# Kernel optimization log

Hardware: AMD Instinct MI355X
Metric: run time of the kernel (lower is better)

Reference implementation:

```python
import jax, jax.numpy as jnp
import numpy as np

NMS_RADIUS = 4   # default_config['nms_radius']
MAX_KP = 256     # default_config['max_keypoints']


def _conv2d(x, w, b):
    y = jax.lax.conv_general_dilated(x, w, (1, 1), [(1, 1), (1, 1)],
                                     dimension_numbers=('NCHW', 'OIHW', 'NCHW'))
    return y + b[None, :, None, None]


def _conv1d(x, w, b, pad):
    y = jax.lax.conv_general_dilated(x, w, (1,), [(pad, pad)],
                                     dimension_numbers=('NCH', 'OIH', 'NCH'))
    return y + b[None, :, None]


def _maxpool(x, r):
    k = 2 * r + 1
    return jax.lax.reduce_window(x, -jnp.inf, jax.lax.max,
                                 (1, k, k), (1, 1, 1), [(0, 0), (r, r), (r, r)])


def _simple_nms(scores, r):
    zeros = jnp.zeros_like(scores)
    max_mask = scores == _maxpool(scores, r)
    for _ in range(2):
        supp_mask = _maxpool(max_mask.astype(scores.dtype), r) > 0
        supp_scores = jnp.where(supp_mask, zeros, scores)
        new_max_mask = supp_scores == _maxpool(supp_scores, r)
        max_mask = max_mask | (new_max_mask & ~supp_mask)
    return jnp.where(max_mask, scores, zeros)


def _affine_grid(theta, H, W):
    # F.affine_grid with align_corners=False
    xs = (jnp.arange(W, dtype=theta.dtype) + 0.5) * (2.0 / W) - 1.0
    ys = (jnp.arange(H, dtype=theta.dtype) + 0.5) * (2.0 / H) - 1.0
    Y, X = jnp.meshgrid(ys, xs, indexing='ij')  # (H, W)
    gx = theta[:, 0, 0, None, None] * X + theta[:, 0, 1, None, None] * Y + theta[:, 0, 2, None, None]
    gy = theta[:, 1, 0, None, None] * X + theta[:, 1, 1, None, None] * Y + theta[:, 1, 2, None, None]
    return jnp.stack([gx, gy], axis=-1)  # (N, H, W, 2)


def _grid_sample(img, grid):
    # F.grid_sample, bilinear, padding_mode='zeros', align_corners=False
    N, C, H, W = img.shape
    ix = ((grid[..., 0] + 1.0) * W - 1.0) * 0.5
    iy = ((grid[..., 1] + 1.0) * H - 1.0) * 0.5
    x0 = jnp.floor(ix); y0 = jnp.floor(iy)
    x1 = x0 + 1.0;      y1 = y0 + 1.0

    def gather(xi, yi):
        valid = (xi >= 0) & (xi <= W - 1) & (yi >= 0) & (yi <= H - 1)
        xc = jnp.clip(xi, 0, W - 1).astype(jnp.int32)
        yc = jnp.clip(yi, 0, H - 1).astype(jnp.int32)
        v = jax.vmap(lambda im, y, x: im[:, y, x])(img, yc, xc)  # (N, C, H, W)
        return v * valid[:, None].astype(img.dtype)

    wa = ((x1 - ix) * (y1 - iy))[:, None]
    wb = ((ix - x0) * (y1 - iy))[:, None]
    wc = ((x1 - ix) * (iy - y0))[:, None]
    wd = ((ix - x0) * (iy - y0))[:, None]
    return (gather(x0, y0) * wa + gather(x1, y0) * wb +
            gather(x0, y1) * wc + gather(x1, y1) * wd)


def setup_inputs() -> dict:
    key = jax.random.key(0)
    ks = jax.random.split(key, 12)
    L, C, H, W = 4, 256, 128, 256
    Cd = C // 2
    s = 0.02
    return {
        'feats':   jax.random.normal(ks[0], (L, C, H, W), jnp.float32),
        'convS_w': jax.random.normal(ks[1], (1, C, 3, 3), jnp.float32) * s,
        'convS_b': jax.random.normal(ks[2], (1,), jnp.float32) * s,
        'convD_w': jax.random.normal(ks[3], (Cd, C, 3, 3), jnp.float32) * s,
        'convD_b': jax.random.normal(ks[4], (Cd,), jnp.float32) * s,
        'proj_w':  jax.random.normal(ks[5], (Cd, Cd, 3), jnp.float32) * s,
        'proj_b':  jax.random.normal(ks[6], (Cd,), jnp.float32) * s,
        'projS_w': jax.random.normal(ks[7], (Cd, Cd, 1), jnp.float32) * s,
        'projS_b': jax.random.normal(ks[8], (Cd,), jnp.float32) * s,
        'final_w': jax.random.normal(ks[9], (3, Cd, 1), jnp.float32) * s,
        'final_b': jax.random.normal(ks[10], (3,), jnp.float32) * s,
    }


def reference(feats, convS_w, convS_b, convD_w, convD_b,
              proj_w, proj_b, projS_w, projS_b, final_w, final_b):
    L, C, H, W = feats.shape
    scores = jax.nn.sigmoid(_conv2d(feats, convS_w, convS_b))[:, 0]   # (L, H, W)
    desc = jax.nn.relu(_conv2d(feats, convD_w, convD_b))               # (L, C//2, H, W)

    scores = _simple_nms(scores, NMS_RADIUS).reshape(L, -1)
    _, top_idx = jax.lax.top_k(scores, MAX_KP)                         # (L, K)

    # F.normalize(p=2, dim=1)
    norm = jnp.sqrt(jnp.sum(desc * desc, axis=1, keepdims=True))
    desc = desc / jnp.maximum(norm, 1e-12)
    desc = desc.reshape(L, desc.shape[1], -1)                          # (L, Cd, HW)
    desc = jnp.take_along_axis(desc, top_idx[:, None, :], axis=2)      # (L, Cd, K)

    # AttentionalGNN: out = desc + (desc + message) = 2*desc + message
    Cd = desc.shape[1]
    qkv = jnp.transpose(desc, (2, 0, 1))                               # (K, L, Cd)
    attn = jnp.einsum('knc,kmc->knm', qkv, qkv) / jnp.sqrt(jnp.asarray(Cd, desc.dtype))
    prob = jax.nn.softmax(attn, axis=-1)
    message = jnp.einsum('knm,kmc->knc', prob, qkv)
    desc = 2.0 * desc + jnp.transpose(message, (1, 2, 0))

    desc = jax.nn.relu(_conv1d(desc, proj_w, proj_b, 1))
    s = _conv1d(desc, projS_w, projS_b, 0)
    order = jnp.argsort(-s, axis=-1)                                   # sort descending per channel
    desc = jnp.take_along_axis(desc, order, axis=-1)
    desc = _conv1d(desc, final_w, final_b, 0)                          # (L, 3, K)
    desc = desc - desc[0:1]

    idx = jnp.argmin(jnp.abs(desc), axis=2, keepdims=True)             # (L, 3, 1)
    picked = jnp.take_along_axis(desc, idx, axis=2)[:, :, 0]           # (L, 3)
    # picked * (picked/|picked|) == picked * sign(picked); sign(0)=0 matches the
    # original's nan->0 replacement for the first (zero-difference) sample.
    min_desc = picked * jnp.sign(picked)
    # the original builds t_matrix from Python floats (math.cos), detaching grads
    min_desc = jax.lax.stop_gradient(min_desc)

    th, tx, ty = min_desc[:, 2], min_desc[:, 0], min_desc[:, 1]
    row0 = jnp.stack([jnp.cos(th), -jnp.sin(th), tx], axis=1)
    row1 = jnp.stack([jnp.sin(th), jnp.cos(th), ty], axis=1)
    theta = jnp.stack([row0, row1], axis=1)                            # (L, 2, 3)

    grid = _affine_grid(theta, H, W)
    return _grid_sample(feats, grid)
```

## Files before the change

### kernel.cpp

```cpp
#include <hip/hip_runtime.h>

#define LIMG 4
#define CIN 256
#define HH 128
#define WW 256
#define HW 32768
#define LHW 131072
#define CD 128
#define KP 256
#define CAP 8192
#define NSP 2
#define CPER (CIN/NSP)
#define NINF -3.402823466e38f

__global__ __launch_bounds__(256) void k_chanred(const float* __restrict__ feats,
                                                 const float* __restrict__ wS,
                                                 float* __restrict__ g,
                                                 const float* __restrict__ wD,
                                                 float* __restrict__ wT,
                                                 int* __restrict__ cnt) {
  int bid = blockIdx.x;
  if (bid >= 1024) {
    int i = (bid - 1024) * 256 + threadIdx.x;
    if (i < LIMG) cnt[i] = 0;
    if (i < CD * CIN * 9) {
      int d = i & (CD - 1);
      int j = i >> 7;
      wT[i] = wD[d * (CIN * 9) + j];
    }
    return;
  }
  int gp   = (bid & 511) * 256 + threadIdx.x;
  int half = bid >> 9;
  int l  = gp >> 15;
  int pi = gp & (HW - 1);
  const float* f = feats + (size_t)(l * CIN + half * CPER) * HW + pi;
  const float* w = wS + half * CPER * 9;
  float a0=0,a1=0,a2=0,a3=0,a4=0,a5=0,a6=0,a7=0,a8=0;
  #pragma unroll 4
  for (int c = 0; c < CPER; ++c) {
    float v = f[(size_t)c * HW];
    const float* wc = w + c * 9;
    a0 = fmaf(wc[0], v, a0); a1 = fmaf(wc[1], v, a1); a2 = fmaf(wc[2], v, a2);
    a3 = fmaf(wc[3], v, a3); a4 = fmaf(wc[4], v, a4); a5 = fmaf(wc[5], v, a5);
    a6 = fmaf(wc[6], v, a6); a7 = fmaf(wc[7], v, a7); a8 = fmaf(wc[8], v, a8);
  }
  float* go = g + (size_t)(half * 9) * LHW + gp;
  go[0*(size_t)LHW]=a0; go[1*(size_t)LHW]=a1; go[2*(size_t)LHW]=a2;
  go[3*(size_t)LHW]=a3; go[4*(size_t)LHW]=a4; go[5*(size_t)LHW]=a5;
  go[6*(size_t)LHW]=a6; go[7*(size_t)LHW]=a7; go[8*(size_t)LHW]=a8;
}

__global__ __launch_bounds__(256) void k_scores(const float* __restrict__ g,
                                                const float* __restrict__ bS,
                                                float* __restrict__ scores) {
  int gp = blockIdx.x * 256 + threadIdx.x;
  int l  = gp >> 15;
  int pi = gp & (HW - 1);
  int y = pi >> 8, x = pi & 255;
  float acc = bS[0];
  #pragma unroll
  for (int ky = 0; ky < 3; ++ky) {
    int yy = y + ky - 1;
    if (yy < 0 || yy >= HH) continue;
    #pragma unroll
    for (int kx = 0; kx < 3; ++kx) {
      int xx = x + kx - 1;
      if (xx < 0 || xx >= WW) continue;
      int tap = ky * 3 + kx;
      size_t q = (size_t)l * HW + yy * WW + xx;
      acc += g[(size_t)tap * LHW + q] + g[(size_t)(9 + tap) * LHW + q];
    }
  }
  scores[gp] = 1.0f / (1.0f + expf(-acc));
}

__global__ __launch_bounds__(256) void k_nms01(const float* __restrict__ scores,
                                               float* __restrict__ maskout) {
  __shared__ float sS[32][152];
  __shared__ float buf[32][152];
  __shared__ float sM[24][144];
  __shared__ float ss[16][136];
  __shared__ float smc[8][128];
  int b = blockIdx.x;
  int l  = b >> 5;
  int yt = (b >> 1) & 15;
  int xt = b & 1;
  int y0 = yt * 8;
  int x0 = xt * 128;
  int tid = threadIdx.x;
  const float* sl = scores + (size_t)l * HW;
  if (tid < 152) {
    int gx = x0 - 12 + tid;
    bool vx = (gx >= 0 && gx < WW);
    for (int r = 0; r < 32; ++r) {
      int gy = y0 - 12 + r;
      sS[r][tid] = (vx && gy >= 0 && gy < HH) ? sl[gy * WW + gx] : NINF;
    }
  }
  __syncthreads();
  if (tid < 144) {
    for (int r = 0; r < 32; ++r) {
      float m = sS[r][tid];
      #pragma unroll
      for (int dx = 1; dx <= 8; ++dx) m = fmaxf(m, sS[r][tid + dx]);
      buf[r][tid] = m;
    }
  }
  __syncthreads();
  if (tid < 144) {
    int gx = x0 - 8 + tid;
    bool vx = (gx >= 0 && gx < WW);
    for (int r3 = 0; r3 < 24; ++r3) {
      int gy = y0 - 8 + r3;
      float m = buf[r3][tid];
      #pragma unroll
      for (int t = 1; t < 9; ++t) m = fmaxf(m, buf[r3 + t][tid]);
      sM[r3][tid] = (vx && gy >= 0 && gy < HH && sS[r3 + 4][tid + 4] == m) ? 1.0f : 0.0f;
    }
  }
  __syncthreads();
  if (tid < 136) {
    for (int r3 = 0; r3 < 24; ++r3) {
      float m = sM[r3][tid];
      #pragma unroll
      for (int dx = 1; dx <= 8; ++dx) m = fmaxf(m, sM[r3][tid + dx]);
      buf[r3][tid] = m;
    }
  }
  __syncthreads();
  if (tid < 136) {
    int gx = x0 - 4 + tid;
    bool vx = (gx >= 0 && gx < WW);
    for (int r2 = 0; r2 < 16; ++r2) {
      int gy = y0 - 4 + r2;
      float m = buf[r2][tid];
      #pragma unroll
      for (int t = 1; t < 9; ++t) m = fmaxf(m, buf[r2 + t][tid]);
      bool sm = m > 0.0f;
      bool vin = vx && gy >= 0 && gy < HH;
      ss[r2][tid] = (sm || !vin) ? 0.0f : sS[r2 + 8][tid + 8];
      if (r2 >= 4 && r2 < 12 && tid >= 4 && tid < 132)
        smc[r2 - 4][tid - 4] = sm ? 1.0f : 0.0f;
    }
  }
  __syncthreads();
  if (tid < 128) {
    for (int r2 = 0; r2 < 16; ++r2) {
      float m = ss[r2][tid];
      #pragma unroll
      for (int dx = 1; dx <= 8; ++dx) m = fmaxf(m, ss[r2][tid + dx]);
      buf[r2][tid] = m;
    }
  }
  __syncthreads();
  if (tid < 128) {
    int gx = x0 + tid;
    for (int r = 0; r < 8; ++r) {
      float m = buf[r][tid];
      #pragma unroll
      for (int t = 1; t < 9; ++t) m = fmaxf(m, buf[r + t][tid]);
      bool nm = (ss[r + 4][tid + 4] == m) && (smc[r][tid] == 0.0f);
      float prev = sM[r + 8][tid + 8];
      maskout[l * HW + (y0 + r) * WW + gx] = (prev != 0.0f || nm) ? 1.0f : 0.0f;
    }
  }
}

__global__ __launch_bounds__(256) void k_nms2(const float* __restrict__ maskin,
                                              const float* __restrict__ scores,
                                              float* __restrict__ maskout,
                                              int* __restrict__ cnt,
                                              int* __restrict__ cidx,
                                              float* __restrict__ csc) {
  __shared__ float m24[24][144];
  __shared__ float buf[24][144];
  __shared__ float ss[16][136];
  __shared__ float smc[8][128];
  int b = blockIdx.x;
  int l  = b >> 5;
  int yt = (b >> 1) & 15;
  int xt = b & 1;
  int y0 = yt * 8;
  int x0 = xt * 128;
  int tid = threadIdx.x;
  const float* ml = maskin + (size_t)l * HW;
  const float* sl = scores + (size_t)l * HW;
  if (tid < 144) {
    int gx = x0 - 8 + tid;
    bool vx = (gx >= 0 && gx < WW);
    for (int r = 0; r < 24; ++r) {
      int gy = y0 - 8 + r;
      m24[r][tid] = (vx && gy >= 0 && gy < HH) ? ml[gy * WW + gx] : 0.0f;
    }
  }
  __syncthreads();
  if (tid < 136) {
    for (int r = 0; r < 24; ++r) {
      float m = m24[r][tid];
      #pragma unroll
      for (int dx = 1; dx <= 8; ++dx) m = fmaxf(m, m24[r][tid + dx]);
      buf[r][tid] = m;
    }
  }
  __syncthreads();
  if (tid < 136) {
    int gx = x0 - 4 + tid;
    bool vx = (gx >= 0 && gx < WW);
    for (int r2 = 0; r2 < 16; ++r2) {
      int gy = y0 - 4 + r2;
      float m = buf[r2][tid];
      #pragma unroll
      for (int t = 1; t < 9; ++t) m = fmaxf(m, buf[r2 + t][tid]);
      bool sm = m > 0.0f;
      bool vin = vx && gy >= 0 && gy < HH;
      ss[r2][tid] = (sm || !vin) ? 0.0f : sl[gy * WW + gx];
      if (r2 >= 4 && r2 < 12 && tid >= 4 && tid < 132)
        smc[r2 - 4][tid - 4] = sm ? 1.0f : 0.0f;
    }
  }
  __syncthreads();
  if (tid < 128) {
    for (int r2 = 0; r2 < 16; ++r2) {
      float m = ss[r2][tid];
      #pragma unroll
      for (int dx = 1; dx <= 8; ++dx) m = fmaxf(m, ss[r2][tid + dx]);
      buf[r2][tid] = m;
    }
  }
  __syncthreads();
  if (tid < 128) {
    int gx = x0 + tid;
    for (int r = 0; r < 8; ++r) {
      float m = buf[r][tid];
      #pragma unroll
      for (int t = 1; t < 9; ++t) m = fmaxf(m, buf[r + t][tid]);
      bool nm = (ss[r + 4][tid + 4] == m) && (smc[r][tid] == 0.0f);
      float prev = m24[r + 8][tid + 8];
      float outv = (prev != 0.0f || nm) ? 1.0f : 0.0f;
      int p = (y0 + r) * WW + gx;
      maskout[l * HW + p] = outv;
      if (outv != 0.0f) {
        int pos = atomicAdd(&cnt[l], 1);
        if (pos < CAP) {
          cidx[l * CAP + pos] = p;
          csc[l * CAP + pos]  = sl[p];
        }
      }
    }
  }
}

__global__ __launch_bounds__(256) void k_rankfill(const int* __restrict__ cnt,
                                                  const int* __restrict__ cidx,
                                                  const float* __restrict__ csc,
                                                  const float* __restrict__ mask,
                                                  int* __restrict__ sel) {
  __shared__ unsigned long long keys[CAP];
  __shared__ int csum[256];
  int b = blockIdx.x;
  int l = b >> 3;
  int tid = threadIdx.x;
  int M = cnt[l]; if (M > CAP) M = CAP;
  const int* ci = cidx + l * CAP;
  const float* cs = csc + l * CAP;
  for (int j = tid; j < M; j += 256) {
    unsigned int ks = __float_as_uint(cs[j]);
    keys[j] = ((unsigned long long)(0xFFFFFFFFu - ks) << 32) | (unsigned int)ci[j];
  }
  __syncthreads();
  for (int i = (b & 7) * 256 + tid; i < M; i += 2048) {
    unsigned long long ki = keys[i];
    int rank = 0;
    for (int j = 0; j < M; ++j)
      rank += (keys[j] < ki) ? 1 : 0;
    if (rank < KP) sel[l * KP + rank] = (int)(unsigned int)(ki & 0xFFFFFFFFu);
  }
  if ((b & 7) != 0) return;
  int Mc = (M < KP) ? M : KP;
  int need = KP - Mc;
  if (need > 0) {
    const float* mk = mask + (size_t)l * HW;
    const int per = HW / 256;
    int base = tid * per;
    int c = 0;
    for (int q = 0; q < per; ++q) c += (mk[base + q] == 0.0f) ? 1 : 0;
    int inc = c;
    csum[tid] = c;
    __syncthreads();
    for (int s = 1; s < 256; s <<= 1) {
      int v = (tid >= s) ? csum[tid - s] : 0;
      __syncthreads();
      csum[tid] += v;
      __syncthreads();
    }
    int excl = csum[tid] - inc;
    if (excl < need) {
      int r = excl;
      for (int q = 0; q < per && r < need; ++q) {
        if (mk[base + q] == 0.0f) { sel[l * KP + Mc + r] = base + q; ++r; }
      }
    }
  }
}

__global__ __launch_bounds__(256) void k_desc1(const float* __restrict__ feats,
                                               const float* __restrict__ wT,
                                               const int* __restrict__ sel,
                                               float* __restrict__ pacc) {
  __shared__ float patch[16][576];
  __shared__ int kpix[16];
  int b = blockIdx.x;
  int q  = b & 3;
  int kb = (b >> 2) & 15;
  int l  = b >> 6;
  int k0 = kb * 16;
  int tid = threadIdx.x;
  if (tid < 16) kpix[tid] = sel[l * KP + k0 + tid];
  __syncthreads();
  int c0 = q * 64;
  for (int e = tid; e < 16 * 576; e += 256) {
    int kp = e / 576;
    int j  = e - kp * 576;
    int c  = j / 9;
    int tap = j - c * 9;
    int ky = tap / 3, kx = tap - ky * 3;
    int pix = kpix[kp];
    int y = pix >> 8, x = pix & 255;
    int yy = y + ky - 1, xx = x + kx - 1;
    float v = 0.0f;
    if (yy >= 0 && yy < HH && xx >= 0 && xx < WW)
      v = feats[((size_t)(l * CIN + c0 + c) * HH + yy) * WW + xx];
    patch[kp][j] = v;
  }
  __syncthreads();
  int d = tid & 127;
  int gg = tid >> 7;
  const float* w = wT + (size_t)(q * 576) * CD + d;
  float a[8] = {0.f,0.f,0.f,0.f,0.f,0.f,0.f,0.f};
  #pragma unroll 2
  for (int j = 0; j < 576; j += 4) {
    float w0 = w[(size_t)(j + 0) * CD];
    float w1 = w[(size_t)(j + 1) * CD];
    float w2 = w[(size_t)(j + 2) * CD];
    float w3 = w[(size_t)(j + 3) * CD];
    #pragma unroll
    for (int i = 0; i < 8; ++i) {
      float4 qv = *(const float4*)&patch[8 * gg + i][j];
      a[i] = fmaf(w0, qv.x, a[i]);
      a[i] = fmaf(w1, qv.y, a[i]);
      a[i] = fmaf(w2, qv.z, a[i]);
      a[i] = fmaf(w3, qv.w, a[i]);
    }
  }
  size_t base = (((size_t)q * LIMG + l) * KP + k0 + 8 * gg) * CD + d;
  #pragma unroll
  for (int i = 0; i < 8; ++i)
    pacc[base + (size_t)i * CD] = a[i];
}

__global__ __launch_bounds__(128) void k_desc2attn(const float* __restrict__ pacc,
                                                   const float* __restrict__ bD,
                                                   float* __restrict__ d2) {
  __shared__ float ps[2][LIMG];
  __shared__ float qs[LIMG][CD];
  __shared__ float dm[16];
  int k = blockIdx.x;
  int d = threadIdx.x;
  float bv = bD[d];
  float r[LIMG];
  #pragma unroll
  for (int l = 0; l < LIMG; ++l) {
    float s = bv;
    #pragma unroll
    for (int qq = 0; qq < 4; ++qq)
      s += pacc[(((size_t)qq * LIMG + l) * KP + k) * CD + d];
    r[l] = fmaxf(s, 0.0f);
  }
  int lane = d & 63, wid = d >> 6;
  #pragma unroll
  for (int l = 0; l < LIMG; ++l) {
    float v = r[l] * r[l];
    #pragma unroll
    for (int sh = 32; sh > 0; sh >>= 1) v += __shfl_down(v, sh);
    if (lane == 0) ps[wid][l] = v;
  }
  __syncthreads();
  float q[LIMG];
  #pragma unroll
  for (int l = 0; l < LIMG; ++l) {
    float n = fmaxf(sqrtf(ps[0][l] + ps[1][l]), 1e-12f);
    q[l] = r[l] / n;
    qs[l][d] = q[l];
  }
  __syncthreads();
  if (d < 16) {
    int n = d >> 2, m = d & 3;
    float s = 0.f;
    for (int t = 0; t < CD; ++t) s = fmaf(qs[n][t], qs[m][t], s);
    dm[d] = s * 0.08838834764831843f;
  }
  __syncthreads();
  #pragma unroll
  for (int n = 0; n < LIMG; ++n) {
    float a0 = dm[n*4+0], a1 = dm[n*4+1], a2 = dm[n*4+2], a3 = dm[n*4+3];
    float mx = fmaxf(fmaxf(a0, a1), fmaxf(a2, a3));
    float e0 = expf(a0 - mx), e1 = expf(a1 - mx), e2 = expf(a2 - mx), e3 = expf(a3 - mx);
    float inv = 1.0f / (e0 + e1 + e2 + e3);
    float msg = (e0 * q[0] + e1 * q[1] + e2 * q[2] + e3 * q[3]) * inv;
    d2[(size_t)(n * CD + d) * KP + k] = 2.0f * q[n] + msg;
  }
}

__global__ __launch_bounds__(256) void k_proj(const float* __restrict__ d2, const float* __restrict__ pw,
                                              const float* __restrict__ pb, float* __restrict__ d3) {
  int b = blockIdx.x;
  int l = b >> 7, o = b & 127;
  int k = threadIdx.x;
  float acc = pb[o];
  for (int c = 0; c < CD; ++c) {
    const float* row = d2 + (size_t)(l * CD + c) * KP;
    float xm = (k > 0)      ? row[k - 1] : 0.f;
    float x0 = row[k];
    float xp = (k < KP - 1) ? row[k + 1] : 0.f;
    const float* w = pw + (size_t)(o * CD + c) * 3;
    acc = fmaf(w[0], xm, acc);
    acc = fmaf(w[1], x0, acc);
    acc = fmaf(w[2], xp, acc);
  }
  d3[(size_t)(l * CD + o) * KP + k] = fmaxf(acc, 0.f);
}

__global__ __launch_bounds__(256) void k_projsort(const float* __restrict__ d3,
                                                  const float* __restrict__ psw,
                                                  const float* __restrict__ psb,
                                                  float* __restrict__ d4) {
  int b = blockIdx.x;
  int l = b >> 7, o = b & 127;
  int k = threadIdx.x;
  __shared__ float srow[KP];
  float acc = psb[o];
  for (int c = 0; c < CD; ++c)
    acc = fmaf(psw[o * CD + c], d3[(size_t)(l * CD + c) * KP + k], acc);
  srow[k] = acc;
  __syncthreads();
  int rank = 0;
  for (int m = 0; m < KP; ++m) {
    float sm = srow[m];
    rank += (sm > acc || (sm == acc && m < k)) ? 1 : 0;
  }
  int base = (l * CD + o) * KP;
  d4[base + rank] = d3[base + k];
}

__global__ __launch_bounds__(1024) void k_finaltheta(const float* __restrict__ d4,
                                                     const float* __restrict__ fw,
                                                     const float* __restrict__ fb,
                                                     float* __restrict__ theta) {
  __shared__ float accs[LIMG][KP][3];
  __shared__ float res[LIMG][3];
  int tid = threadIdx.x;
  int l = tid >> 8, k = tid & 255;
  float a0 = fb[0], a1 = fb[1], a2 = fb[2];
  const float* dl = d4 + (size_t)l * CD * KP + k;
  for (int c = 0; c < CD; ++c) {
    float v = dl[(size_t)c * KP];
    a0 = fmaf(fw[0 * CD + c], v, a0);
    a1 = fmaf(fw[1 * CD + c], v, a1);
    a2 = fmaf(fw[2 * CD + c], v, a2);
  }
  accs[l][k][0] = a0; accs[l][k][1] = a1; accs[l][k][2] = a2;
  __syncthreads();
  int wid = tid >> 6, lane = tid & 63;
  if (wid < 12) {
    int rl = wid / 3, ro = wid - rl * 3;
    float m = 3.402823466e38f;
    #pragma unroll
    for (int t = 0; t < 4; ++t) {
      int kk = lane + 64 * t;
      m = fminf(m, fabsf(accs[rl][kk][ro] - accs[0][kk][ro]));
    }
    #pragma unroll
    for (int s = 32; s > 0; s >>= 1) m = fminf(m, __shfl_down(m, s));
    if (lane == 0) res[rl][ro] = m;
  }
  __syncthreads();
  if (tid == 0) {
    for (int l2 = 0; l2 < LIMG; ++l2) {
      float tx = res[l2][0], ty = res[l2][1], th = res[l2][2];
      float cth = cosf(th), sth = sinf(th);
      theta[l2*6+0] = cth;  theta[l2*6+1] = -sth; theta[l2*6+2] = tx;
      theta[l2*6+3] = sth;  theta[l2*6+4] = cth;  theta[l2*6+5] = ty;
    }
  }
}

__global__ __launch_bounds__(256) void k_sample(const float* __restrict__ feats,
                                                const float* __restrict__ theta,
                                                float* __restrict__ out) {
  int b = blockIdx.x;
  int pb = b & 127;
  int cg = (b >> 7) & 31;
  int l  = b >> 12;
  int pi = pb * 256 + threadIdx.x;
  int x = pi & 255, y = pi >> 8;
  const float* t = theta + l * 6;
  float X = (x + 0.5f) * (2.0f / WW) - 1.0f;
  float Y = (y + 0.5f) * (2.0f / HH) - 1.0f;
  float gx = t[0] * X + t[1] * Y + t[2];
  float gy = t[3] * X + t[4] * Y + t[5];
  float ix = ((gx + 1.0f) * WW - 1.0f) * 0.5f;
  float iy = ((gy + 1.0f) * HH - 1.0f) * 0.5f;
  float x0 = floorf(ix), y0 = floorf(iy);
  float x1 = x0 + 1.0f,  y1 = y0 + 1.0f;
  float wa = (x1 - ix) * (y1 - iy);
  float wb = (ix - x0) * (y1 - iy);
  float wc = (x1 - ix) * (iy - y0);
  float wd = (ix - x0) * (iy - y0);
  bool vx0 = (x0 >= 0.f) && (x0 <= (float)(WW-1));
  bool vx1 = (x1 >= 0.f) && (x1 <= (float)(WW-1));
  bool vy0 = (y0 >= 0.f) && (y0 <= (float)(HH-1));
  bool vy1 = (y1 >= 0.f) && (y1 <= (float)(HH-1));
  wa = (vx0 && vy0) ? wa : 0.f;
  wb = (vx1 && vy0) ? wb : 0.f;
  wc = (vx0 && vy1) ? wc : 0.f;
  wd = (vx1 && vy1) ? wd : 0.f;
  int xc0 = (int)fminf(fmaxf(x0, 0.f), (float)(WW-1));
  int xc1 = (int)fminf(fmaxf(x1, 0.f), (float)(WW-1));
  int yc0 = (int)fminf(fmaxf(y0, 0.f), (float)(HH-1));
  int yc1 = (int)fminf(fmaxf(y1, 0.f), (float)(HH-1));
  int o00 = yc0 * WW + xc0;
  int o10 = yc0 * WW + xc1;
  int o01 = yc1 * WW + xc0;
  int o11 = yc1 * WW + xc1;
  const float* img = feats + (size_t)(l * CIN + cg * 8) * HW;
  float* op = out + (size_t)(l * CIN + cg * 8) * HW + pi;
  #pragma unroll
  for (int i = 0; i < 8; ++i) {
    const float* im = img + (size_t)i * HW;
    float acc = im[o00] * wa + im[o10] * wb + im[o01] * wc + im[o11] * wd;
    op[(size_t)i * HW] = acc;
  }
}

extern "C" void kernel_launch(void* const* d_in, const int* in_sizes, int n_in,
                              void* d_out, int out_size, void* d_ws, size_t ws_size,
                              hipStream_t stream) {
  const float* feats = (const float*)d_in[0];
  const float* wS    = (const float*)d_in[1];
  const float* bS    = (const float*)d_in[2];
  const float* wD    = (const float*)d_in[3];
  const float* bD    = (const float*)d_in[4];
  const float* pw    = (const float*)d_in[5];
  const float* pb    = (const float*)d_in[6];
  const float* psw   = (const float*)d_in[7];
  const float* psb   = (const float*)d_in[8];
  const float* fw    = (const float*)d_in[9];
  const float* fb    = (const float*)d_in[10];
  float* out = (float*)d_out;

  char* base = (char*)d_ws;
  size_t off = 0;
  auto alloc = [&](size_t bytes) -> void* {
    void* p = base + off;
    off = (off + bytes + 255) & ~(size_t)255;
    return p;
  };
  float* g      = (float*)alloc((size_t)NSP * 9 * LHW * sizeof(float));
  float* scores = (float*)alloc((size_t)LHW * 4);
  float* maskA  = (float*)alloc((size_t)LHW * 4);
  float* maskB  = (float*)alloc((size_t)LHW * 4);
  float* d2     = (float*)alloc((size_t)LHW * 4);
  float* d3     = (float*)alloc((size_t)LHW * 4);
  float* d4     = (float*)alloc((size_t)LHW * 4);
  float* wT     = (float*)alloc((size_t)CIN * 9 * CD * 4);
  float* pacc   = (float*)alloc((size_t)4 * LIMG * KP * CD * 4);
  float* theta  = (float*)alloc(24 * 4);
  float* csc    = (float*)alloc((size_t)LIMG * CAP * 4);
  int*   cidx   = (int*)  alloc((size_t)LIMG * CAP * 4);
  int*   cnt    = (int*)  alloc(64);
  int*   sel    = (int*)  alloc((size_t)LIMG * KP * 4);

  const int WT_BLOCKS = (CD * CIN * 9 + 255) / 256;
  k_chanred<<<1024 + WT_BLOCKS, 256, 0, stream>>>(feats, wS, g, wD, wT, cnt);
  k_scores<<<512, 256, 0, stream>>>(g, bS, scores);
  k_nms01<<<128, 256, 0, stream>>>(scores, maskA);
  k_nms2<<<128, 256, 0, stream>>>(maskA, scores, maskB, cnt, cidx, csc);
  k_rankfill<<<32, 256, 0, stream>>>(cnt, cidx, csc, maskB, sel);
  k_desc1<<<256, 256, 0, stream>>>(feats, wT, sel, pacc);
  k_desc2attn<<<256, 128, 0, stream>>>(pacc, bD, d2);
  k_proj<<<512, 256, 0, stream>>>(d2, pw, pb, d3);
  k_projsort<<<512, 256, 0, stream>>>(d3, psw, psb, d4);
  k_finaltheta<<<1, 1024, 0, stream>>>(d4, fw, fb, theta);
  k_sample<<<16384, 256, 0, stream>>>(feats, theta, out);
}
```

Measured before the change: 235.3 us.

## Fuse post-reduction pipeline stages into one cooperative persistent kernel with grid syncs

Replaces the ten kernel launches after the channel reduction with a single cooperative kernel of 256 blocks. It walks through scores, NMS, ranking, descriptor, attention, projection, sort, theta and sampling stages, separated by grid.sync(). The aim is to remove per-launch overhead and the tail idle time between the many small kernels. In exchange, the heavy sampling stage runs on only 256 persistent blocks, and each grid-wide barrier costs time. The old launch sequence is kept as a fallback if the cooperative launch fails.

```diff
diff --git a/kernel.cpp b/kernel.cpp
--- a/kernel.cpp
+++ b/kernel.cpp
@@ -1,4 +1,7 @@
 #include <hip/hip_runtime.h>
+#include <hip/hip_cooperative_groups.h>
+
+namespace cg = cooperative_groups;
 
 #define LIMG 4
 #define CIN 256
@@ -49,6 +52,492 @@
   go[0*(size_t)LHW]=a0; go[1*(size_t)LHW]=a1; go[2*(size_t)LHW]=a2;
   go[3*(size_t)LHW]=a3; go[4*(size_t)LHW]=a4; go[5*(size_t)LHW]=a5;
   go[6*(size_t)LHW]=a6; go[7*(size_t)LHW]=a7; go[8*(size_t)LHW]=a8;
+}
+
+union Smem {
+  struct { float sS[32][152], buf[32][152], sM[24][144], ss[16][136], smc[8][128]; } n1;
+  struct { float m24[24][144], buf[24][144], ss[16][136], smc[8][128]; } n2;
+  unsigned long long keys[CAP];
+  struct { float patch[16][576]; int kpix[16]; } d1;
+  struct { float ps[2][LIMG]; float qs[LIMG][CD]; float dm[16]; } at;
+  float srow[KP];
+  struct { float sv[256]; float res[LIMG][3]; } ft;
+};
+
+__global__ __launch_bounds__(256) void k_mega(
+    const float* __restrict__ feats, const float* __restrict__ g,
+    const float* __restrict__ bS, float* __restrict__ scores,
+    float* __restrict__ maskA, float* __restrict__ maskB,
+    int* __restrict__ cnt, int* __restrict__ cidx, float* __restrict__ csc,
+    int* __restrict__ sel, const float* __restrict__ wT,
+    const float* __restrict__ bD, float* __restrict__ pacc,
+    float* __restrict__ d2, const float* __restrict__ pw,
+    const float* __restrict__ pb, float* __restrict__ d3,
+    const float* __restrict__ psw, const float* __restrict__ psb,
+    float* __restrict__ d4, const float* __restrict__ fw,
+    const float* __restrict__ fb, float* __restrict__ theta,
+    float* __restrict__ out) {
+  cg::grid_group grid = cg::this_grid();
+  __shared__ Smem sm;
+  __shared__ int csum[256];
+  const int bid = blockIdx.x;
+  const int tid = threadIdx.x;
+
+  for (int u = bid; u < 512; u += 256) {
+    int gp = u * 256 + tid;
+    int l  = gp >> 15;
+    int pi = gp & (HW - 1);
+    int y = pi >> 8, x = pi & 255;
+    float acc = bS[0];
+    #pragma unroll
+    for (int ky = 0; ky < 3; ++ky) {
+      int yy = y + ky - 1;
+      if (yy < 0 || yy >= HH) continue;
+      #pragma unroll
+      for (int kx = 0; kx < 3; ++kx) {
+        int xx = x + kx - 1;
+        if (xx < 0 || xx >= WW) continue;
+        int tap = ky * 3 + kx;
+        size_t q = (size_t)l * HW + yy * WW + xx;
+        acc += g[(size_t)tap * LHW + q] + g[(size_t)(9 + tap) * LHW + q];
+      }
+    }
+    scores[gp] = 1.0f / (1.0f + expf(-acc));
+  }
+  grid.sync();
+
+  if (bid < 128) {
+    int l  = bid >> 5;
+    int yt = (bid >> 1) & 15;
+    int xt = bid & 1;
+    int y0 = yt * 8;
+    int x0 = xt * 128;
+    const float* sl = scores + (size_t)l * HW;
+    if (tid < 152) {
+      int gx = x0 - 12 + tid;
+      bool vx = (gx >= 0 && gx < WW);
+      for (int r = 0; r < 32; ++r) {
+        int gy = y0 - 12 + r;
+        sm.n1.sS[r][tid] = (vx && gy >= 0 && gy < HH) ? sl[gy * WW + gx] : NINF;
+      }
+    }
+    __syncthreads();
+    if (tid < 144) {
+      for (int r = 0; r < 32; ++r) {
+        float m = sm.n1.sS[r][tid];
+        #pragma unroll
+        for (int dx = 1; dx <= 8; ++dx) m = fmaxf(m, sm.n1.sS[r][tid + dx]);
+        sm.n1.buf[r][tid] = m;
+      }
+    }
+    __syncthreads();
+    if (tid < 144) {
+      int gx = x0 - 8 + tid;
+      bool vx = (gx >= 0 && gx < WW);
+      for (int r3 = 0; r3 < 24; ++r3) {
+        int gy = y0 - 8 + r3;
+        float m = sm.n1.buf[r3][tid];
+        #pragma unroll
+        for (int t = 1; t < 9; ++t) m = fmaxf(m, sm.n1.buf[r3 + t][tid]);
+        sm.n1.sM[r3][tid] = (vx && gy >= 0 && gy < HH && sm.n1.sS[r3 + 4][tid + 4] == m) ? 1.0f : 0.0f;
+      }
+    }
+    __syncthreads();
+    if (tid < 136) {
+      for (int r3 = 0; r3 < 24; ++r3) {
+        float m = sm.n1.sM[r3][tid];
+        #pragma unroll
+        for (int dx = 1; dx <= 8; ++dx) m = fmaxf(m, sm.n1.sM[r3][tid + dx]);
+        sm.n1.buf[r3][tid] = m;
+      }
+    }
+    __syncthreads();
+    if (tid < 136) {
+      int gx = x0 - 4 + tid;
+      bool vx = (gx >= 0 && gx < WW);
+      for (int r2 = 0; r2 < 16; ++r2) {
+        int gy = y0 - 4 + r2;
+        float m = sm.n1.buf[r2][tid];
+        #pragma unroll
+        for (int t = 1; t < 9; ++t) m = fmaxf(m, sm.n1.buf[r2 + t][tid]);
+        bool smv = m > 0.0f;
+        bool vin = vx && gy >= 0 && gy < HH;
+        sm.n1.ss[r2][tid] = (smv || !vin) ? 0.0f : sm.n1.sS[r2 + 8][tid + 8];
+        if (r2 >= 4 && r2 < 12 && tid >= 4 && tid < 132)
+          sm.n1.smc[r2 - 4][tid - 4] = smv ? 1.0f : 0.0f;
+      }
+    }
+    __syncthreads();
+    if (tid < 128) {
+      for (int r2 = 0; r2 < 16; ++r2) {
+        float m = sm.n1.ss[r2][tid];
+        #pragma unroll
+        for (int dx = 1; dx <= 8; ++dx) m = fmaxf(m, sm.n1.ss[r2][tid + dx]);
+        sm.n1.buf[r2][tid] = m;
+      }
+    }
+    __syncthreads();
+    if (tid < 128) {
+      int gx = x0 + tid;
+      for (int r = 0; r < 8; ++r) {
+        float m = sm.n1.buf[r][tid];
+        #pragma unroll
+        for (int t = 1; t < 9; ++t) m = fmaxf(m, sm.n1.buf[r + t][tid]);
+        bool nm = (sm.n1.ss[r + 4][tid + 4] == m) && (sm.n1.smc[r][tid] == 0.0f);
+        float prev = sm.n1.sM[r + 8][tid + 8];
+        maskA[l * HW + (y0 + r) * WW + gx] = (prev != 0.0f || nm) ? 1.0f : 0.0f;
+      }
+    }
+  }
+  grid.sync();
+
+  if (bid < 128) {
+    int l  = bid >> 5;
+    int yt = (bid >> 1) & 15;
+    int xt = bid & 1;
+    int y0 = yt * 8;
+    int x0 = xt * 128;
+    const float* ml = maskA + (size_t)l * HW;
+    const float* sl = scores + (size_t)l * HW;
+    if (tid < 144) {
+      int gx = x0 - 8 + tid;
+      bool vx = (gx >= 0 && gx < WW);
+      for (int r = 0; r < 24; ++r) {
+        int gy = y0 - 8 + r;
+        sm.n2.m24[r][tid] = (vx && gy >= 0 && gy < HH) ? ml[gy * WW + gx] : 0.0f;
+      }
+    }
+    __syncthreads();
+    if (tid < 136) {
+      for (int r = 0; r < 24; ++r) {
+        float m = sm.n2.m24[r][tid];
+        #pragma unroll
+        for (int dx = 1; dx <= 8; ++dx) m = fmaxf(m, sm.n2.m24[r][tid + dx]);
+        sm.n2.buf[r][tid] = m;
+      }
+    }
+    __syncthreads();
+    if (tid < 136) {
+      int gx = x0 - 4 + tid;
+      bool vx = (gx >= 0 && gx < WW);
+      for (int r2 = 0; r2 < 16; ++r2) {
+        int gy = y0 - 4 + r2;
+        float m = sm.n2.buf[r2][tid];
+        #pragma unroll
+        for (int t = 1; t < 9; ++t) m = fmaxf(m, sm.n2.buf[r2 + t][tid]);
+        bool smv = m > 0.0f;
+        bool vin = vx && gy >= 0 && gy < HH;
+        sm.n2.ss[r2][tid] = (smv || !vin) ? 0.0f : sl[gy * WW + gx];
+        if (r2 >= 4 && r2 < 12 && tid >= 4 && tid < 132)
+          sm.n2.smc[r2 - 4][tid - 4] = smv ? 1.0f : 0.0f;
+      }
+    }
+    __syncthreads();
+    if (tid < 128) {
+      for (int r2 = 0; r2 < 16; ++r2) {
+        float m = sm.n2.ss[r2][tid];
+        #pragma unroll
+        for (int dx = 1; dx <= 8; ++dx) m = fmaxf(m, sm.n2.ss[r2][tid + dx]);
+        sm.n2.buf[r2][tid] = m;
+      }
+    }
+    __syncthreads();
+    if (tid < 128) {
+      int gx = x0 + tid;
+      for (int r = 0; r < 8; ++r) {
+        float m = sm.n2.buf[r][tid];
+        #pragma unroll
+        for (int t = 1; t < 9; ++t) m = fmaxf(m, sm.n2.buf[r + t][tid]);
+        bool nm = (sm.n2.ss[r + 4][tid + 4] == m) && (sm.n2.smc[r][tid] == 0.0f);
+        float prev = sm.n2.m24[r + 8][tid + 8];
+        float outv = (prev != 0.0f || nm) ? 1.0f : 0.0f;
+        int p = (y0 + r) * WW + gx;
+        maskB[l * HW + p] = outv;
+        if (outv != 0.0f) {
+          int pos = atomicAdd(&cnt[l], 1);
+          if (pos < CAP) {
+            cidx[l * CAP + pos] = p;
+            csc[l * CAP + pos]  = sl[p];
+          }
+        }
+      }
+    }
+  }
+  grid.sync();
+
+  if (bid < 32) {
+    int l = bid >> 3;
+    int M = cnt[l]; if (M > CAP) M = CAP;
+    const int* ci = cidx + l * CAP;
+    const float* cs = csc + l * CAP;
+    for (int j = tid; j < M; j += 256) {
+      unsigned int ks = __float_as_uint(cs[j]);
+      sm.keys[j] = ((unsigned long long)(0xFFFFFFFFu - ks) << 32) | (unsigned int)ci[j];
+    }
+    __syncthreads();
+    for (int i = (bid & 7) * 256 + tid; i < M; i += 2048) {
+      unsigned long long ki = sm.keys[i];
+      int rank = 0;
+      for (int j = 0; j < M; ++j)
+        rank += (sm.keys[j] < ki) ? 1 : 0;
+      if (rank < KP) sel[l * KP + rank] = (int)(unsigned int)(ki & 0xFFFFFFFFu);
+    }
+    if ((bid & 7) == 0) {
+      int Mc = (M < KP) ? M : KP;
+      int need = KP - Mc;
+      if (need > 0) {
+        const float* mk = maskB + (size_t)l * HW;
+        const int per = HW / 256;
+        int base = tid * per;
+        int c = 0;
+        for (int q = 0; q < per; ++q) c += (mk[base + q] == 0.0f) ? 1 : 0;
+        int inc = c;
+        csum[tid] = c;
+        __syncthreads();
+        for (int s = 1; s < 256; s <<= 1) {
+          int v = (tid >= s) ? csum[tid - s] : 0;
+          __syncthreads();
+          csum[tid] += v;
+          __syncthreads();
+        }
+        int excl = csum[tid] - inc;
+        if (excl < need) {
+          int r = excl;
+          for (int q = 0; q < per && r < need; ++q) {
+            if (mk[base + q] == 0.0f) { sel[l * KP + Mc + r] = base + q; ++r; }
+          }
+        }
+      }
+    }
+  }
+  grid.sync();
+
+  {
+    int q  = bid & 3;
+    int kb = (bid >> 2) & 15;
+    int l  = bid >> 6;
+    int k0 = kb * 16;
+    if (tid < 16) sm.d1.kpix[tid] = sel[l * KP + k0 + tid];
+    __syncthreads();
+    int c0 = q * 64;
+    for (int e = tid; e < 16 * 576; e += 256) {
+      int kp = e / 576;
+      int j  = e - kp * 576;
+      int c  = j / 9;
+      int tap = j - c * 9;
+      int ky = tap / 3, kx = tap - ky * 3;
+      int pix = sm.d1.kpix[kp];
+      int y = pix >> 8, x = pix & 255;
+      int yy = y + ky - 1, xx = x + kx - 1;
+      float v = 0.0f;
+      if (yy >= 0 && yy < HH && xx >= 0 && xx < WW)
+        v = feats[((size_t)(l * CIN + c0 + c) * HH + yy) * WW + xx];
+      sm.d1.patch[kp][j] = v;
+    }
+    __syncthreads();
+    int d = tid & 127;
+    int gg = tid >> 7;
+    const float* w = wT + (size_t)(q * 576) * CD + d;
+    float a[8] = {0.f,0.f,0.f,0.f,0.f,0.f,0.f,0.f};
+    #pragma unroll 2
+    for (int j = 0; j < 576; j += 4) {
+      float w0 = w[(size_t)(j + 0) * CD];
+      float w1 = w[(size_t)(j + 1) * CD];
+      float w2 = w[(size_t)(j + 2) * CD];
+      float w3 = w[(size_t)(j + 3) * CD];
+      #pragma unroll
+      for (int i = 0; i < 8; ++i) {
+        float4 qv = *(const float4*)&sm.d1.patch[8 * gg + i][j];
+        a[i] = fmaf(w0, qv.x, a[i]);
+        a[i] = fmaf(w1, qv.y, a[i]);
+        a[i] = fmaf(w2, qv.z, a[i]);
+        a[i] = fmaf(w3, qv.w, a[i]);
+      }
+    }
+    size_t pbase = (((size_t)q * LIMG + l) * KP + k0 + 8 * gg) * CD + d;
+    #pragma unroll
+    for (int i = 0; i < 8; ++i)
+      pacc[pbase + (size_t)i * CD] = a[i];
+  }
+  grid.sync();
+
+  {
+    int k = bid;
+    int d = tid;
+    bool act = d < 128;
+    float r[LIMG], q[LIMG];
+    if (act) {
+      float bv = bD[d];
+      #pragma unroll
+      for (int l = 0; l < LIMG; ++l) {
+        float s = bv;
+        #pragma unroll
+        for (int qq = 0; qq < 4; ++qq)
+          s += pacc[(((size_t)qq * LIMG + l) * KP + k) * CD + d];
+        r[l] = fmaxf(s, 0.0f);
+      }
+      int lane = d & 63, wid = d >> 6;
+      #pragma unroll
+      for (int l = 0; l < LIMG; ++l) {
+        float v = r[l] * r[l];
+        #pragma unroll
+        for (int sh = 32; sh > 0; sh >>= 1) v += __shfl_down(v, sh);
+        if (lane == 0) sm.at.ps[wid][l] = v;
+      }
+    }
+    __syncthreads();
+    if (act) {
+      #pragma unroll
+      for (int l = 0; l < LIMG; ++l) {
+        float n = fmaxf(sqrtf(sm.at.ps[0][l] + sm.at.ps[1][l]), 1e-12f);
+        q[l] = r[l] / n;
+        sm.at.qs[l][d] = q[l];
+      }
+    }
+    __syncthreads();
+    if (tid < 16) {
+      int n = tid >> 2, m = tid & 3;
+      float s = 0.f;
+      for (int t = 0; t < CD; ++t) s = fmaf(sm.at.qs[n][t], sm.at.qs[m][t], s);
+      sm.at.dm[tid] = s * 0.08838834764831843f;
+    }
+    __syncthreads();
+    if (act) {
+      #pragma unroll
+      for (int n = 0; n < LIMG; ++n) {
+        float a0 = sm.at.dm[n*4+0], a1 = sm.at.dm[n*4+1];
+        float a2 = sm.at.dm[n*4+2], a3 = sm.at.dm[n*4+3];
+        float mx = fmaxf(fmaxf(a0, a1), fmaxf(a2, a3));
+        float e0 = expf(a0 - mx), e1 = expf(a1 - mx), e2 = expf(a2 - mx), e3 = expf(a3 - mx);
+        float inv = 1.0f / (e0 + e1 + e2 + e3);
+        float msg = (e0 * q[0] + e1 * q[1] + e2 * q[2] + e3 * q[3]) * inv;
+        d2[(size_t)(n * CD + d) * KP + k] = 2.0f * q[n] + msg;
+      }
+    }
+  }
+  grid.sync();
+
+  for (int u = bid; u < 512; u += 256) {
+    int l = u >> 7, o = u & 127;
+    int k = tid;
+    float acc = pb[o];
+    for (int c = 0; c < CD; ++c) {
+      const float* row = d2 + (size_t)(l * CD + c) * KP;
+      float xm = (k > 0)      ? row[k - 1] : 0.f;
+      float x0 = row[k];
+      float xp = (k < KP - 1) ? row[k + 1] : 0.f;
+      const float* w = pw + (size_t)(o * CD + c) * 3;
+      acc = fmaf(w[0], xm, acc);
+      acc = fmaf(w[1], x0, acc);
+      acc = fmaf(w[2], xp, acc);
+    }
+    d3[(size_t)(l * CD + o) * KP + k] = fmaxf(acc, 0.f);
+  }
+  grid.sync();
+
+  for (int u = bid; u < 512; u += 256) {
+    int l = u >> 7, o = u & 127;
+    int k = tid;
+    float acc = psb[o];
+    for (int c = 0; c < CD; ++c)
+      acc = fmaf(psw[o * CD + c], d3[(size_t)(l * CD + c) * KP + k], acc);
+    __syncthreads();
+    sm.srow[k] = acc;
+    __syncthreads();
+    int rank = 0;
+    for (int m = 0; m < KP; ++m) {
+      float smv = sm.srow[m];
+      rank += (smv > acc || (smv == acc && m < k)) ? 1 : 0;
+    }
+    int base = (l * CD + o) * KP;
+    d4[base + rank] = d3[base + k];
+  }
+  grid.sync();
+
+  if (bid == 0) {
+    int k = tid;
+    float acc[LIMG][3];
+    #pragma unroll
+    for (int l = 0; l < LIMG; ++l)
+      #pragma unroll
+      for (int o = 0; o < 3; ++o) acc[l][o] = fb[o];
+    for (int c = 0; c < CD; ++c) {
+      float w0 = fw[0 * CD + c], w1 = fw[1 * CD + c], w2 = fw[2 * CD + c];
+      #pragma unroll
+      for (int l = 0; l < LIMG; ++l) {
+        float v = d4[(size_t)(l * CD + c) * KP + k];
+        acc[l][0] = fmaf(w0, v, acc[l][0]);
+        acc[l][1] = fmaf(w1, v, acc[l][1]);
+        acc[l][2] = fmaf(w2, v, acc[l][2]);
+      }
+    }
+    for (int l = 0; l < LIMG; ++l) {
+      for (int o = 0; o < 3; ++o) {
+        sm.ft.sv[k] = fabsf(acc[l][o] - acc[0][o]);
+        __syncthreads();
+        for (int s = 128; s > 0; s >>= 1) {
+          if (k < s) sm.ft.sv[k] = fminf(sm.ft.sv[k], sm.ft.sv[k + s]);
+          __syncthreads();
+        }
+        if (k == 0) sm.ft.res[l][o] = sm.ft.sv[0];
+        __syncthreads();
+      }
+    }
+    if (k == 0) {
+      for (int l2 = 0; l2 < LIMG; ++l2) {
+        float tx = sm.ft.res[l2][0], ty = sm.ft.res[l2][1], th = sm.ft.res[l2][2];
+        float cth = cosf(th), sth = sinf(th);
+        theta[l2*6+0] = cth;  theta[l2*6+1] = -sth; theta[l2*6+2] = tx;
+        theta[l2*6+3] = sth;  theta[l2*6+4] = cth;  theta[l2*6+5] = ty;
+      }
+    }
+  }
+  grid.sync();
+
+  for (int u = bid; u < 16384; u += 256) {
+    int pb2 = u & 127;
+    int cg2 = (u >> 7) & 31;
+    int l   = u >> 12;
+    int pi = pb2 * 256 + tid;
+    int x = pi & 255, y = pi >> 8;
+    const float* t = theta + l * 6;
+    float X = (x + 0.5f) * (2.0f / WW) - 1.0f;
+    float Y = (y + 0.5f) * (2.0f / HH) - 1.0f;
+    float gx = t[0] * X + t[1] * Y + t[2];
+    float gy = t[3] * X + t[4] * Y + t[5];
+    float ix = ((gx + 1.0f) * WW - 1.0f) * 0.5f;
+    float iy = ((gy + 1.0f) * HH - 1.0f) * 0.5f;
+    float x0 = floorf(ix), y0 = floorf(iy);
+    float x1 = x0 + 1.0f,  y1 = y0 + 1.0f;
+    float wa = (x1 - ix) * (y1 - iy);
+    float wb = (ix - x0) * (y1 - iy);
+    float wc = (x1 - ix) * (iy - y0);
+    float wd = (ix - x0) * (iy - y0);
+    bool vx0 = (x0 >= 0.f) && (x0 <= (float)(WW-1));
+    bool vx1 = (x1 >= 0.f) && (x1 <= (float)(WW-1));
+    bool vy0 = (y0 >= 0.f) && (y0 <= (float)(HH-1));
+    bool vy1 = (y1 >= 0.f) && (y1 <= (float)(HH-1));
+    wa = (vx0 && vy0) ? wa : 0.f;
+    wb = (vx1 && vy0) ? wb : 0.f;
+    wc = (vx0 && vy1) ? wc : 0.f;
+    wd = (vx1 && vy1) ? wd : 0.f;
+    int xc0 = (int)fminf(fmaxf(x0, 0.f), (float)(WW-1));
+    int xc1 = (int)fminf(fmaxf(x1, 0.f), (float)(WW-1));
+    int yc0 = (int)fminf(fmaxf(y0, 0.f), (float)(HH-1));
+    int yc1 = (int)fminf(fmaxf(y1, 0.f), (float)(HH-1));
+    int o00 = yc0 * WW + xc0;
+    int o10 = yc0 * WW + xc1;
+    int o01 = yc1 * WW + xc0;
+    int o11 = yc1 * WW + xc1;
+    const float* img = feats + (size_t)(l * CIN + cg2 * 8) * HW;
+    float* op = out + (size_t)(l * CIN + cg2 * 8) * HW + pi;
+    #pragma unroll
+    for (int i = 0; i < 8; ++i) {
+      const float* im = img + (size_t)i * HW;
+      float acc = im[o00] * wa + im[o10] * wb + im[o01] * wc + im[o11] * wd;
+      op[(size_t)i * HW] = acc;
+    }
+  }
 }
 
 __global__ __launch_bounds__(256) void k_scores(const float* __restrict__ g,
@@ -500,7 +989,7 @@
                                                 float* __restrict__ out) {
   int b = blockIdx.x;
   int pb = b & 127;
-  int cg = (b >> 7) & 31;
+  int cg2 = (b >> 7) & 31;
   int l  = b >> 12;
   int pi = pb * 256 + threadIdx.x;
   int x = pi & 255, y = pi >> 8;
@@ -533,8 +1022,8 @@
   int o10 = yc0 * WW + xc1;
   int o01 = yc1 * WW + xc0;
   int o11 = yc1 * WW + xc1;
-  const float* img = feats + (size_t)(l * CIN + cg * 8) * HW;
-  float* op = out + (size_t)(l * CIN + cg * 8) * HW + pi;
+  const float* img = feats + (size_t)(l * CIN + cg2 * 8) * HW;
+  float* op = out + (size_t)(l * CIN + cg2 * 8) * HW + pi;
   #pragma unroll
   for (int i = 0; i < 8; ++i) {
     const float* im = img + (size_t)i * HW;
@@ -583,14 +1072,26 @@
 
   const int WT_BLOCKS = (CD * CIN * 9 + 255) / 256;
   k_chanred<<<1024 + WT_BLOCKS, 256, 0, stream>>>(feats, wS, g, wD, wT, cnt);
-  k_scores<<<512, 256, 0, stream>>>(g, bS, scores);
-  k_nms01<<<128, 256, 0, stream>>>(scores, maskA);
-  k_nms2<<<128, 256, 0, stream>>>(maskA, scores, maskB, cnt, cidx, csc);
-  k_rankfill<<<32, 256, 0, stream>>>(cnt, cidx, csc, maskB, sel);
-  k_desc1<<<256, 256, 0, stream>>>(feats, wT, sel, pacc);
-  k_desc2attn<<<256, 128, 0, stream>>>(pacc, bD, d2);
-  k_proj<<<512, 256, 0, stream>>>(d2, pw, pb, d3);
-  k_projsort<<<512, 256, 0, stream>>>(d3, psw, psb, d4);
-  k_finaltheta<<<1, 1024, 0, stream>>>(d4, fw, fb, theta);
-  k_sample<<<16384, 256, 0, stream>>>(feats, theta, out);
-}
+
+  void* args[] = { (void*)&feats, (void*)&g, (void*)&bS, (void*)&scores,
+                   (void*)&maskA, (void*)&maskB, (void*)&cnt, (void*)&cidx,
+                   (void*)&csc, (void*)&sel, (void*)&wT, (void*)&bD,
+                   (void*)&pacc, (void*)&d2, (void*)&pw, (void*)&pb,
+                   (void*)&d3, (void*)&psw, (void*)&psb, (void*)&d4,
+                   (void*)&fw, (void*)&fb, (void*)&theta, (void*)&out };
+  hipError_t err = hipLaunchCooperativeKernel((void*)k_mega, dim3(256), dim3(256),
+                                              args, 0, stream);
+  if (err != hipSuccess) {
+    (void)hipGetLastError();
+    k_scores<<<512, 256, 0, stream>>>(g, bS, scores);
+    k_nms01<<<128, 256, 0, stream>>>(scores, maskA);
+    k_nms2<<<128, 256, 0, stream>>>(maskA, scores, maskB, cnt, cidx, csc);
+    k_rankfill<<<32, 256, 0, stream>>>(cnt, cidx, csc, maskB, sel);
+    k_desc1<<<256, 256, 0, stream>>>(feats, wT, sel, pacc);
+    k_desc2attn<<<256, 128, 0, stream>>>(pacc, bD, d2);
+    k_proj<<<512, 256, 0, stream>>>(d2, pw, pb, d3);
+    k_projsort<<<512, 256, 0, stream>>>(d3, psw, psb, d4);
+    k_finaltheta<<<1, 1024, 0, stream>>>(d4, fw, fb, theta);
+    k_sample<<<16384, 256, 0, stream>>>(feats, theta, out);
+  }
+}
```

After: 517.8 us. 2.2x slower.
